# Optimization experiments

Hardware: AMD Instinct MI355X
Metric: run time of the kernel (lower is better)

The kernel has to match this reference:

```python
import jax, jax.numpy as jnp
import numpy as np

N, E, G = 20000, 400000, 200
IN, HID, OUT, H = 8, 64, 32, 4
EPS = 1e-5
NEG_SLOPE = 0.2


def _gatv2(x, src, dst, Wl, bl, Wr, br, att, bias, n, heads, c):
    # lin_l (source messages) and lin_r (target queries)
    xl = (x @ Wl + bl).reshape(n, heads, c)
    xr = (x @ Wr + br).reshape(n, heads, c)
    # per-edge GATv2 score: att . LeakyReLU(x_l[j] + x_r[i])
    e = jax.nn.leaky_relu(xl[src] + xr[dst], NEG_SLOPE)          # [E,H,C]
    score = jnp.einsum('ehc,hc->eh', e, att)                     # [E,H]
    # softmax over incoming edges of each target node
    m = jax.ops.segment_max(score, dst, num_segments=n)
    ex = jnp.exp(score - m[dst])
    den = jax.ops.segment_sum(ex, dst, num_segments=n)
    alpha = ex / den[dst]                                        # [E,H]
    out = jax.ops.segment_sum(alpha[:, :, None] * xl[src], dst, num_segments=n)
    return out.mean(axis=1) + bias                               # concat=False: head mean


def _layernorm(x, g, b):
    mu = x.mean(-1, keepdims=True)
    var = ((x - mu) ** 2).mean(-1, keepdims=True)
    return (x - mu) * jax.lax.rsqrt(var + EPS) * g + b


def setup_inputs() -> dict:
    key = jax.random.key(0)
    ks = jax.random.split(key, 16)
    s = 0.1
    inp = {
        'x': jax.random.normal(ks[0], (N, IN), jnp.float32),
        'edge_index': jax.random.randint(ks[1], (2, E), 0, N, jnp.int64 if jax.config.jax_enable_x64 else jnp.int32),
        'batch': jnp.sort(jax.random.randint(ks[2], (N,), 0, G)),
        'Wl1': jax.random.normal(ks[3], (IN, H * HID), jnp.float32) * s,
        'bl1': jnp.zeros((H * HID,), jnp.float32),
        'Wr1': jax.random.normal(ks[4], (IN, H * HID), jnp.float32) * s,
        'br1': jnp.zeros((H * HID,), jnp.float32),
        'att1': jax.random.normal(ks[5], (H, HID), jnp.float32) * s,
        'b1': jnp.zeros((HID,), jnp.float32),
        'ln1_g': jnp.ones((HID,), jnp.float32),
        'ln1_b': jnp.zeros((HID,), jnp.float32),
        'Wl2': jax.random.normal(ks[6], (HID, H * OUT), jnp.float32) * s,
        'bl2': jnp.zeros((H * OUT,), jnp.float32),
        'Wr2': jax.random.normal(ks[7], (HID, H * OUT), jnp.float32) * s,
        'br2': jnp.zeros((H * OUT,), jnp.float32),
        'att2': jax.random.normal(ks[8], (H, OUT), jnp.float32) * s,
        'b2': jnp.zeros((OUT,), jnp.float32),
        'ln2_g': jnp.ones((OUT,), jnp.float32),
        'ln2_b': jnp.zeros((OUT,), jnp.float32),
    }
    return inp


def reference(x, edge_index, batch, Wl1, bl1, Wr1, br1, att1, b1, ln1_g, ln1_b,
              Wl2, bl2, Wr2, br2, att2, b2, ln2_g, ln2_b):
    n = x.shape[0]
    loop = jnp.arange(n, dtype=edge_index.dtype)  # add_self_loops=True (PyG default)
    src = jnp.concatenate([edge_index[0], loop])
    dst = jnp.concatenate([edge_index[1], loop])

    h = _gatv2(x, src, dst, Wl1, bl1, Wr1, br1, att1, b1, n, H, HID)
    h = jax.nn.relu(_layernorm(h, ln1_g, ln1_b))
    h = _gatv2(h, src, dst, Wl2, bl2, Wr2, br2, att2, b2, n, H, OUT)
    h = jax.nn.relu(_layernorm(h, ln2_g, ln2_b))

    # global mean pool per graph
    cnt = jax.ops.segment_sum(jnp.ones((n,), h.dtype), batch, num_segments=G)
    pooled = jax.ops.segment_sum(h, batch, num_segments=G)
    return pooled / jnp.maximum(cnt, 1.0)[:, None]
```

## Files before the change

### kernel.cpp

```cpp
#include <hip/hip_runtime.h>
#include <math.h>
#include <stdint.h>

#define NEG_SLOPE 0.2f
#define LN_EPS 1e-5f

typedef __attribute__((ext_vector_type(8))) short short8;
typedef __attribute__((ext_vector_type(4))) float f32x4;

__device__ __forceinline__ uint32_t pack_bf2(float a, float b) {
  uint32_t ua = __float_as_uint(a);
  uint32_t ub = __float_as_uint(b);
  ua = (ua + 0x7fffu + ((ua >> 16) & 1u)) >> 16;
  ub = (ub + 0x7fffu + ((ub >> 16) & 1u)) & 0xffff0000u;
  return ua | ub;
}
__device__ __forceinline__ float2 unpack_bf2(uint32_t u) {
  return make_float2(__uint_as_float(u << 16), __uint_as_float(u & 0xffff0000u));
}
__device__ __forceinline__ uint16_t bf16_rne(float f) {
  uint32_t u = __float_as_uint(f);
  return (uint16_t)((u + 0x7fffu + ((u >> 16) & 1u)) >> 16);
}

__device__ __forceinline__ float row16_sum(float x) {
  x += __int_as_float(__builtin_amdgcn_mov_dpp(__float_as_int(x), 0xB1, 0xF, 0xF, true));
  x += __int_as_float(__builtin_amdgcn_mov_dpp(__float_as_int(x), 0x4E, 0xF, 0xF, true));
  x += __int_as_float(__builtin_amdgcn_mov_dpp(__float_as_int(x), 0x124, 0xF, 0xF, true));
  x += __int_as_float(__builtin_amdgcn_mov_dpp(__float_as_int(x), 0x128, 0xF, 0xF, true));
  return x;
}

__global__ void zero_kernel(int* __restrict__ p, int n) {
  int i = blockIdx.x * blockDim.x + threadIdx.x;
  if (i < n) p[i] = 0;
}

__global__ __launch_bounds__(256) void gemm1_hist_kernel(
    const float* __restrict__ x,
    const float* __restrict__ Wl, const float* __restrict__ bl,
    const float* __restrict__ Wr, const float* __restrict__ br,
    uint32_t* __restrict__ xl1b, float* __restrict__ xr1, int N,
    const int* __restrict__ ei, int E, int* __restrict__ cnt) {
  int tid = threadIdx.x;
  int c2 = tid & 127;
  int which = tid >> 7;
  float wl0[8], wl1[8], wr0[8], wr1[8];
#pragma unroll
  for (int k = 0; k < 8; ++k) {
    wl0[k] = Wl[k * 256 + 2 * c2]; wl1[k] = Wl[k * 256 + 2 * c2 + 1];
    wr0[k] = Wr[k * 256 + 2 * c2]; wr1[k] = Wr[k * 256 + 2 * c2 + 1];
  }
  float bl0 = bl[2 * c2], bl1v = bl[2 * c2 + 1];
  float br0 = br[2 * c2], br1v = br[2 * c2 + 1];
  int npair = (N + 1) >> 1;
  for (int pr = blockIdx.x; pr < npair; pr += gridDim.x) {
    int n = pr * 2 + which;
    if (n >= N) continue;
    float4 xa = ((const float4*)x)[n * 2];
    float4 xb = ((const float4*)x)[n * 2 + 1];
    float xs[8] = {xa.x, xa.y, xa.z, xa.w, xb.x, xb.y, xb.z, xb.w};
    float al0 = bl0, al1 = bl1v, ar0 = br0, ar1 = br1v;
#pragma unroll
    for (int k = 0; k < 8; ++k) {
      al0 = fmaf(xs[k], wl0[k], al0); al1 = fmaf(xs[k], wl1[k], al1);
      ar0 = fmaf(xs[k], wr0[k], ar0); ar1 = fmaf(xs[k], wr1[k], ar1);
    }
    xl1b[(size_t)n * 128 + c2] = pack_bf2(al0, al1);
    ((float2*)xr1)[(size_t)n * 128 + c2] = make_float2(ar0, ar1);
  }
  int tot = E + N;
  for (int e = blockIdx.x * blockDim.x + tid; e < tot; e += gridDim.x * blockDim.x) {
    int dst = (e < E) ? ei[E + e] : (e - E);
    atomicAdd(&cnt[dst], 1);
  }
}

__global__ __launch_bounds__(1024) void scan_kernel(const int* __restrict__ cnt,
                                                    int* __restrict__ offs,
                                                    int* __restrict__ cursor, int n) {
  __shared__ int wsum[16];
  int tid = threadIdx.x;
  int lane = tid & 63, w = tid >> 6;
  int PER = (n + 1023) >> 10;
  int base = tid * PER;
  int s = 0;
  for (int j = 0; j < PER; ++j) {
    int idx = base + j;
    s += (idx < n) ? cnt[idx] : 0;
  }
  int inc = s;
#pragma unroll
  for (int d = 1; d < 64; d <<= 1) {
    int t = __shfl_up(inc, d, 64);
    if (lane >= d) inc += t;
  }
  if (lane == 63) wsum[w] = inc;
  __syncthreads();
  int wpre = 0;
  for (int j = 0; j < w; ++j) wpre += wsum[j];
  int run = wpre + inc - s;
  for (int j = 0; j < PER; ++j) {
    int idx = base + j;
    if (idx < n) {
      offs[idx] = run;
      cursor[idx] = run;
      run += cnt[idx];
    }
  }
  if (tid == 1023) offs[n] = run;
}

__global__ void scatter_kernel(const int* __restrict__ ei, int E, int N,
                               int* __restrict__ cursor, int* __restrict__ esrc,
                               const float* __restrict__ Wl2, const float* __restrict__ Wr2,
                               uint16_t* __restrict__ Wtb) {
  if (blockIdx.x < 64) {
    int idx = blockIdx.x * 256 + threadIdx.x;
    int c = idx >> 6, k = idx & 63;
    float v = (c < 128) ? Wl2[k * 128 + c] : Wr2[k * 128 + (c - 128)];
    Wtb[idx] = bf16_rne(v);
  }
  int e = blockIdx.x * blockDim.x + threadIdx.x;
  if (e >= E + N) return;
  int src, dst;
  if (e < E) { src = ei[e]; dst = ei[E + e]; }
  else       { src = e - E; dst = src; }
  int pos = atomicAdd(&cursor[dst], 1);
  esrc[pos] = src;
}

__global__ __launch_bounds__(256) void gemm2_mfma_kernel(
    const uint16_t* __restrict__ h1b,
    const uint16_t* __restrict__ Wtb,
    const float* __restrict__ bl, const float* __restrict__ br,
    uint32_t* __restrict__ xl2b, float* __restrict__ xr2, int N) {
  int lane = threadIdx.x & 63;
  int w = threadIdx.x >> 6;
  int c0 = w << 6;
  int l15 = lane & 15, l4 = lane >> 4;
  int node = (blockIdx.x << 4) + l15;
  int nodec = node < N ? node : N - 1;
  const short8* hrow = (const short8*)(h1b + (size_t)nodec * 64);
  short8 b0 = hrow[l4];
  short8 b1 = hrow[4 + l4];
  f32x4 acc[4] = {{0.f,0.f,0.f,0.f},{0.f,0.f,0.f,0.f},{0.f,0.f,0.f,0.f},{0.f,0.f,0.f,0.f}};
#pragma unroll
  for (int t = 0; t < 4; ++t) {
    int row = c0 + (t << 4) + l15;
    const short8* wrow = (const short8*)(Wtb + (size_t)row * 64);
    short8 a0 = wrow[l4];
    short8 a1 = wrow[4 + l4];
    acc[t] = __builtin_amdgcn_mfma_f32_16x16x32_bf16(a0, b0, acc[t], 0, 0, 0);
    acc[t] = __builtin_amdgcn_mfma_f32_16x16x32_bf16(a1, b1, acc[t], 0, 0, 0);
  }
  if (node >= N) return;
  if (c0 < 128) {
#pragma unroll
    for (int t = 0; t < 4; ++t) {
      int q0 = c0 + (t << 4) + (l4 << 2);
      float4 bb = *(const float4*)(bl + q0);
      uint2 pk;
      pk.x = pack_bf2(acc[t][0] + bb.x, acc[t][1] + bb.y);
      pk.y = pack_bf2(acc[t][2] + bb.z, acc[t][3] + bb.w);
      *(uint2*)(xl2b + (size_t)node * 64 + (q0 >> 1)) = pk;
    }
  } else {
#pragma unroll
    for (int t = 0; t < 4; ++t) {
      int q0 = (c0 - 128) + (t << 4) + (l4 << 2);
      float4 bb = *(const float4*)(br + q0);
      float4 v = make_float4(acc[t][0] + bb.x, acc[t][1] + bb.y,
                             acc[t][2] + bb.z, acc[t][3] + bb.w);
      *(float4*)(xr2 + (size_t)node * 128 + q0) = v;
    }
  }
}

__global__ __launch_bounds__(256) void attn1_kernel(
    const uint32_t* __restrict__ xl1b, const float* __restrict__ xr1,
    const float* __restrict__ att, const float* __restrict__ b1,
    const float* __restrict__ g, const float* __restrict__ be,
    const int* __restrict__ offs, const int* __restrict__ esrc,
    uint32_t* __restrict__ h1b, int N) {
  const float L2E = 1.4426950408889634f;
  int lane = threadIdx.x & 63;
  int i = blockIdx.x * (blockDim.x >> 6) + (threadIdx.x >> 6);
  if (i >= N) return;
  int cq = lane & 15;
  const uint2* xlb = (const uint2*)xl1b;
  float4 attq = ((const float4*)att)[lane];
  float4 a4 = make_float4(0.4f * L2E * attq.x, 0.4f * L2E * attq.y,
                          0.4f * L2E * attq.z, 0.4f * L2E * attq.w);
  float4 xrq = ((const float4*)xr1)[(size_t)i * 64 + lane];
  float dA = 0.f, aA0 = 0.f, aA1 = 0.f, aA2 = 0.f, aA3 = 0.f;
  float dB = 0.f, aB0 = 0.f, aB1 = 0.f, aB2 = 0.f, aB3 = 0.f;
  int beg = offs[i], end = offs[i + 1];
  int p = beg;

#define EDGE1(U, DD, A0, A1, A2, A3)                                           \
  {                                                                            \
    float2 e0 = unpack_bf2(U.x), e1 = unpack_bf2(U.y);                         \
    float t0 = e0.x + xrq.x, t1 = e0.y + xrq.y;                                \
    float t2 = e1.x + xrq.z, t3 = e1.y + xrq.w;                                \
    float u0 = fmaf(1.5f, t0, fabsf(t0));                                      \
    float u1 = fmaf(1.5f, t1, fabsf(t1));                                      \
    float u2 = fmaf(1.5f, t2, fabsf(t2));                                      \
    float u3 = fmaf(1.5f, t3, fabsf(t3));                                      \
    float sc = a4.x * u0;                                                      \
    sc = fmaf(a4.y, u1, sc);                                                   \
    sc = fmaf(a4.z, u2, sc);                                                   \
    sc = fmaf(a4.w, u3, sc);                                                   \
    sc = row16_sum(sc);                                                        \
    float wgt = exp2f(sc);                                                     \
    DD += wgt;                                                                 \
    A0 = fmaf(wgt, e0.x, A0); A1 = fmaf(wgt, e0.y, A1);                        \
    A2 = fmaf(wgt, e1.x, A2); A3 = fmaf(wgt, e1.y, A3);                        \
  }

  for (; p + 3 < end; p += 4) {
    int s0 = __builtin_amdgcn_readfirstlane(esrc[p]);
    int s1 = __builtin_amdgcn_readfirstlane(esrc[p + 1]);
    int s2 = __builtin_amdgcn_readfirstlane(esrc[p + 2]);
    int s3 = __builtin_amdgcn_readfirstlane(esrc[p + 3]);
    uint2 u0 = (xlb + (size_t)s0 * 64)[lane];
    uint2 u1 = (xlb + (size_t)s1 * 64)[lane];
    uint2 u2 = (xlb + (size_t)s2 * 64)[lane];
    uint2 u3 = (xlb + (size_t)s3 * 64)[lane];
    EDGE1(u0, dA, aA0, aA1, aA2, aA3)
    EDGE1(u1, dB, aB0, aB1, aB2, aB3)
    EDGE1(u2, dA, aA0, aA1, aA2, aA3)
    EDGE1(u3, dB, aB0, aB1, aB2, aB3)
  }
  for (; p < end; ++p) {
    int s0 = __builtin_amdgcn_readfirstlane(esrc[p]);
    uint2 u0 = (xlb + (size_t)s0 * 64)[lane];
    EDGE1(u0, dA, aA0, aA1, aA2, aA3)
  }
#undef EDGE1

  float inv = 1.0f / (dA + dB);
  float v0 = (aA0 + aB0) * inv;
  float v1 = (aA1 + aB1) * inv;
  float v2 = (aA2 + aB2) * inv;
  float v3 = (aA3 + aB3) * inv;
  v0 += __shfl_xor(v0, 16, 64); v0 += __shfl_xor(v0, 32, 64);
  v1 += __shfl_xor(v1, 16, 64); v1 += __shfl_xor(v1, 32, 64);
  v2 += __shfl_xor(v2, 16, 64); v2 += __shfl_xor(v2, 32, 64);
  v3 += __shfl_xor(v3, 16, 64); v3 += __shfl_xor(v3, 32, 64);
  float4 b1q = ((const float4*)b1)[cq];
  v0 = 0.25f * v0 + b1q.x;
  v1 = 0.25f * v1 + b1q.y;
  v2 = 0.25f * v2 + b1q.z;
  v3 = 0.25f * v3 + b1q.w;
  float s1 = row16_sum(v0 + v1 + v2 + v3);
  float mu = s1 * (1.0f / 64.0f);
  float d0 = v0 - mu, d1 = v1 - mu, d2 = v2 - mu, d3 = v3 - mu;
  float s2 = row16_sum(d0 * d0 + d1 * d1 + d2 * d2 + d3 * d3);
  float rstd = rsqrtf(s2 * (1.0f / 64.0f) + LN_EPS);
  float4 gq = ((const float4*)g)[cq];
  float4 beq = ((const float4*)be)[cq];
  float y0 = fmaxf(fmaf(d0 * rstd, gq.x, beq.x), 0.f);
  float y1 = fmaxf(fmaf(d1 * rstd, gq.y, beq.y), 0.f);
  float y2 = fmaxf(fmaf(d2 * rstd, gq.z, beq.z), 0.f);
  float y3 = fmaxf(fmaf(d3 * rstd, gq.w, beq.w), 0.f);
  if (lane < 16) {
    uint2 pk;
    pk.x = pack_bf2(y0, y1);
    pk.y = pack_bf2(y2, y3);
    *(uint2*)(h1b + (size_t)i * 32 + cq * 2) = pk;
  }
}

__global__ __launch_bounds__(256) void attn2_kernel(
    const uint32_t* __restrict__ xl2b, const float* __restrict__ xr2,
    const float* __restrict__ att, const float* __restrict__ b2,
    const float* __restrict__ g, const float* __restrict__ be,
    const int* __restrict__ offs, const int* __restrict__ esrc,
    float* __restrict__ h2, int N) {
  const float L2E = 1.4426950408889634f;
  int lane = threadIdx.x & 63;
  int i = blockIdx.x * (blockDim.x >> 6) + (threadIdx.x >> 6);
  if (i >= N) return;
  int cq = lane & 15;
  float2 attq = ((const float2*)att)[lane];
  float2 a4 = make_float2(0.4f * L2E * attq.x, 0.4f * L2E * attq.y);
  float2 xrq = ((const float2*)xr2)[(size_t)i * 64 + lane];
  float dA = 0.f, aA0 = 0.f, aA1 = 0.f;
  float dB = 0.f, aB0 = 0.f, aB1 = 0.f;
  int beg = offs[i], end = offs[i + 1];
  int p = beg;

#define EDGE2(U, DD, A0, A1)                                                   \
  {                                                                            \
    float2 e0 = unpack_bf2(U);                                                 \
    float t0 = e0.x + xrq.x, t1 = e0.y + xrq.y;                                \
    float u0 = fmaf(1.5f, t0, fabsf(t0));                                      \
    float u1 = fmaf(1.5f, t1, fabsf(t1));                                      \
    float sc = fmaf(a4.y, u1, a4.x * u0);                                      \
    sc = row16_sum(sc);                                                        \
    float wgt = exp2f(sc);                                                     \
    DD += wgt;                                                                 \
    A0 = fmaf(wgt, e0.x, A0); A1 = fmaf(wgt, e0.y, A1);                        \
  }

  for (; p + 3 < end; p += 4) {
    int s0 = __builtin_amdgcn_readfirstlane(esrc[p]);
    int s1 = __builtin_amdgcn_readfirstlane(esrc[p + 1]);
    int s2 = __builtin_amdgcn_readfirstlane(esrc[p + 2]);
    int s3 = __builtin_amdgcn_readfirstlane(esrc[p + 3]);
    uint32_t u0 = (xl2b + (size_t)s0 * 64)[lane];
    uint32_t u1 = (xl2b + (size_t)s1 * 64)[lane];
    uint32_t u2 = (xl2b + (size_t)s2 * 64)[lane];
    uint32_t u3 = (xl2b + (size_t)s3 * 64)[lane];
    EDGE2(u0, dA, aA0, aA1)
    EDGE2(u1, dB, aB0, aB1)
    EDGE2(u2, dA, aA0, aA1)
    EDGE2(u3, dB, aB0, aB1)
  }
  for (; p < end; ++p) {
    int s0 = __builtin_amdgcn_readfirstlane(esrc[p]);
    uint32_t u0 = (xl2b + (size_t)s0 * 64)[lane];
    EDGE2(u0, dA, aA0, aA1)
  }
#undef EDGE2

  float inv = 1.0f / (dA + dB);
  float v0 = (aA0 + aB0) * inv;
  float v1 = (aA1 + aB1) * inv;
  v0 += __shfl_xor(v0, 16, 64); v0 += __shfl_xor(v0, 32, 64);
  v1 += __shfl_xor(v1, 16, 64); v1 += __shfl_xor(v1, 32, 64);
  float2 b2q = ((const float2*)b2)[cq];
  v0 = 0.25f * v0 + b2q.x;
  v1 = 0.25f * v1 + b2q.y;
  float s1 = row16_sum(v0 + v1);
  float mu = s1 * (1.0f / 32.0f);
  float d0 = v0 - mu, d1 = v1 - mu;
  float s2 = row16_sum(d0 * d0 + d1 * d1);
  float rstd = rsqrtf(s2 * (1.0f / 32.0f) + LN_EPS);
  float2 gq = ((const float2*)g)[cq];
  float2 beq = ((const float2*)be)[cq];
  float y0 = fmaxf(fmaf(d0 * rstd, gq.x, beq.x), 0.f);
  float y1 = fmaxf(fmaf(d1 * rstd, gq.y, beq.y), 0.f);
  if (lane < 16) ((float2*)h2)[(size_t)i * 16 + cq] = make_float2(y0, y1);
}

__global__ __launch_bounds__(256) void pool_kernel(const float* __restrict__ h2,
                                                   const int* __restrict__ batch,
                                                   float* __restrict__ out, int N) {
  int gidx = blockIdx.x;
  int a = 0, b = N;
  while (a < b) { int m = (a + b) >> 1; if (batch[m] < gidx) a = m + 1; else b = m; }
  int lo = a;
  b = N;
  while (a < b) { int m = (a + b) >> 1; if (batch[m] < gidx + 1) a = m + 1; else b = m; }
  int hi = a;
  int c = threadIdx.x & 31, r = threadIdx.x >> 5;
  float s = 0.f;
  for (int n = lo + r; n < hi; n += 8) s += h2[(size_t)n * 32 + c];
  __shared__ float buf[256];
  buf[threadIdx.x] = s;
  __syncthreads();
  if (threadIdx.x < 128) buf[threadIdx.x] += buf[threadIdx.x + 128];
  __syncthreads();
  if (threadIdx.x < 64) buf[threadIdx.x] += buf[threadIdx.x + 64];
  __syncthreads();
  if (threadIdx.x < 32) {
    float v = buf[threadIdx.x] + buf[threadIdx.x + 32];
    int cnt = hi - lo;
    out[gidx * 32 + threadIdx.x] = v / (float)(cnt > 0 ? cnt : 1);
  }
}

extern "C" void kernel_launch(void* const* d_in, const int* in_sizes, int n_in,
                              void* d_out, int out_size, void* d_ws, size_t ws_size,
                              hipStream_t stream) {
  const float* x    = (const float*)d_in[0];
  const int*   ei   = (const int*)d_in[1];
  const int*   batch= (const int*)d_in[2];
  const float* Wl1  = (const float*)d_in[3];
  const float* bl1  = (const float*)d_in[4];
  const float* Wr1  = (const float*)d_in[5];
  const float* br1  = (const float*)d_in[6];
  const float* att1 = (const float*)d_in[7];
  const float* b1   = (const float*)d_in[8];
  const float* ln1g = (const float*)d_in[9];
  const float* ln1b = (const float*)d_in[10];
  const float* Wl2  = (const float*)d_in[11];
  const float* bl2  = (const float*)d_in[12];
  const float* Wr2  = (const float*)d_in[13];
  const float* br2  = (const float*)d_in[14];
  const float* att2 = (const float*)d_in[15];
  const float* b2   = (const float*)d_in[16];
  const float* ln2g = (const float*)d_in[17];
  const float* ln2b = (const float*)d_in[18];

  int N = in_sizes[0] / 8;
  int E = in_sizes[1] / 2;
  int G = out_size / 32;

  char* ws = (char*)d_ws;
  size_t off = 0;
  auto alloc = [&](size_t bytes) -> void* {
    void* p = (void*)(ws + off);
    off += (bytes + 255) & ~(size_t)255;
    return p;
  };
  int*      cnt    = (int*)alloc((size_t)N * 4);
  int*      offs   = (int*)alloc((size_t)(N + 1) * 4);
  int*      cursor = (int*)alloc((size_t)N * 4);
  int*      esrc   = (int*)alloc((size_t)(E + N) * 4);
  uint32_t* xl1b   = (uint32_t*)alloc((size_t)N * 128 * 4);
  float*    xr1    = (float*)alloc((size_t)N * 256 * 4);
  uint32_t* h1b    = (uint32_t*)alloc((size_t)N * 64 * 2);
  uint16_t* Wtb    = (uint16_t*)alloc((size_t)256 * 64 * 2);
  uint32_t* xl2b   = (uint32_t*)alloc((size_t)N * 64 * 4);
  float*    xr2    = (float*)alloc((size_t)N * 128 * 4);
  float*    h2     = (float*)alloc((size_t)N * 32 * 4);

  int tot = E + N;
  zero_kernel<<<(N + 255) / 256, 256, 0, stream>>>(cnt, N);
  gemm1_hist_kernel<<<2048, 256, 0, stream>>>(x, Wl1, bl1, Wr1, br1, xl1b, xr1, N,
                                              ei, E, cnt);
  scan_kernel<<<1, 1024, 0, stream>>>(cnt, offs, cursor, N);
  scatter_kernel<<<(tot + 255) / 256, 256, 0, stream>>>(ei, E, N, cursor, esrc,
                                                        Wl2, Wr2, Wtb);

  attn1_kernel<<<(N + 3) / 4, 256, 0, stream>>>(xl1b, xr1, att1, b1, ln1g, ln1b,
                                                offs, esrc, h1b, N);
  gemm2_mfma_kernel<<<(N + 15) / 16, 256, 0, stream>>>((const uint16_t*)h1b, Wtb, bl2, br2,
                                                       xl2b, xr2, N);
  attn2_kernel<<<(N + 3) / 4, 256, 0, stream>>>(xl2b, xr2, att2, b2, ln2g, ln2b,
                                                offs, esrc, h2, N);

  pool_kernel<<<G, 256, 0, stream>>>(h2, batch, (float*)d_out, N);
}
```

Baseline: 175.8 us.

## Fuse layer-1 projection into attention gather and pool via atomics

```diff
diff --git a/kernel.cpp b/kernel.cpp
--- a/kernel.cpp
+++ b/kernel.cpp
@@ -36,44 +36,11 @@
   if (i < n) p[i] = 0;
 }
 
-__global__ __launch_bounds__(256) void gemm1_hist_kernel(
-    const float* __restrict__ x,
-    const float* __restrict__ Wl, const float* __restrict__ bl,
-    const float* __restrict__ Wr, const float* __restrict__ br,
-    uint32_t* __restrict__ xl1b, float* __restrict__ xr1, int N,
-    const int* __restrict__ ei, int E, int* __restrict__ cnt) {
-  int tid = threadIdx.x;
-  int c2 = tid & 127;
-  int which = tid >> 7;
-  float wl0[8], wl1[8], wr0[8], wr1[8];
-#pragma unroll
-  for (int k = 0; k < 8; ++k) {
-    wl0[k] = Wl[k * 256 + 2 * c2]; wl1[k] = Wl[k * 256 + 2 * c2 + 1];
-    wr0[k] = Wr[k * 256 + 2 * c2]; wr1[k] = Wr[k * 256 + 2 * c2 + 1];
-  }
-  float bl0 = bl[2 * c2], bl1v = bl[2 * c2 + 1];
-  float br0 = br[2 * c2], br1v = br[2 * c2 + 1];
-  int npair = (N + 1) >> 1;
-  for (int pr = blockIdx.x; pr < npair; pr += gridDim.x) {
-    int n = pr * 2 + which;
-    if (n >= N) continue;
-    float4 xa = ((const float4*)x)[n * 2];
-    float4 xb = ((const float4*)x)[n * 2 + 1];
-    float xs[8] = {xa.x, xa.y, xa.z, xa.w, xb.x, xb.y, xb.z, xb.w};
-    float al0 = bl0, al1 = bl1v, ar0 = br0, ar1 = br1v;
-#pragma unroll
-    for (int k = 0; k < 8; ++k) {
-      al0 = fmaf(xs[k], wl0[k], al0); al1 = fmaf(xs[k], wl1[k], al1);
-      ar0 = fmaf(xs[k], wr0[k], ar0); ar1 = fmaf(xs[k], wr1[k], ar1);
-    }
-    xl1b[(size_t)n * 128 + c2] = pack_bf2(al0, al1);
-    ((float2*)xr1)[(size_t)n * 128 + c2] = make_float2(ar0, ar1);
-  }
-  int tot = E + N;
-  for (int e = blockIdx.x * blockDim.x + tid; e < tot; e += gridDim.x * blockDim.x) {
-    int dst = (e < E) ? ei[E + e] : (e - E);
-    atomicAdd(&cnt[dst], 1);
-  }
+__global__ void hist_kernel(const int* __restrict__ ei, int E, int N, int* __restrict__ cnt) {
+  int e = blockIdx.x * blockDim.x + threadIdx.x;
+  if (e >= E + N) return;
+  int dst = (e < E) ? ei[E + e] : (e - E);
+  atomicAdd(&cnt[dst], 1);
 }
 
 __global__ __launch_bounds__(1024) void scan_kernel(const int* __restrict__ cnt,
@@ -178,7 +145,9 @@
 }
 
 __global__ __launch_bounds__(256) void attn1_kernel(
-    const uint32_t* __restrict__ xl1b, const float* __restrict__ xr1,
+    const float* __restrict__ x,
+    const float* __restrict__ Wl, const float* __restrict__ bl,
+    const float* __restrict__ Wr, const float* __restrict__ br,
     const float* __restrict__ att, const float* __restrict__ b1,
     const float* __restrict__ g, const float* __restrict__ be,
     const int* __restrict__ offs, const int* __restrict__ esrc,
@@ -188,25 +157,50 @@
   int i = blockIdx.x * (blockDim.x >> 6) + (threadIdx.x >> 6);
   if (i >= N) return;
   int cq = lane & 15;
-  const uint2* xlb = (const uint2*)xl1b;
+  const float4* xf4 = (const float4*)x;
+  float4 wl[8];
+#pragma unroll
+  for (int k = 0; k < 8; ++k) wl[k] = ((const float4*)(Wl + k * 256))[lane];
   float4 attq = ((const float4*)att)[lane];
   float4 a4 = make_float4(0.4f * L2E * attq.x, 0.4f * L2E * attq.y,
                           0.4f * L2E * attq.z, 0.4f * L2E * attq.w);
-  float4 xrq = ((const float4*)xr1)[(size_t)i * 64 + lane];
-  float dA = 0.f, aA0 = 0.f, aA1 = 0.f, aA2 = 0.f, aA3 = 0.f;
-  float dB = 0.f, aB0 = 0.f, aB1 = 0.f, aB2 = 0.f, aB3 = 0.f;
+  float4 xa = xf4[(size_t)i * 2], xbv = xf4[(size_t)i * 2 + 1];
+  float xs[8] = {xa.x, xa.y, xa.z, xa.w, xbv.x, xbv.y, xbv.z, xbv.w};
+  float4 xr = ((const float4*)br)[lane];
+#pragma unroll
+  for (int k = 0; k < 8; ++k) {
+    float4 wr = ((const float4*)(Wr + k * 256))[lane];
+    xr.x = fmaf(xs[k], wr.x, xr.x);
+    xr.y = fmaf(xs[k], wr.y, xr.y);
+    xr.z = fmaf(xs[k], wr.z, xr.z);
+    xr.w = fmaf(xs[k], wr.w, xr.w);
+  }
+  float4 tb = ((const float4*)bl)[lane];
+  tb.x += xr.x; tb.y += xr.y; tb.z += xr.z; tb.w += xr.w;
+
+  float dA = 0.f, dB = 0.f;
+  float4 accA = make_float4(0.f, 0.f, 0.f, 0.f);
+  float4 accB = make_float4(0.f, 0.f, 0.f, 0.f);
   int beg = offs[i], end = offs[i + 1];
   int p = beg;
 
-#define EDGE1(U, DD, A0, A1, A2, A3)                                           \
+#define EDGE1(XA, XB, DD, ACC)                                                 \
   {                                                                            \
-    float2 e0 = unpack_bf2(U.x), e1 = unpack_bf2(U.y);                         \
-    float t0 = e0.x + xrq.x, t1 = e0.y + xrq.y;                                \
-    float t2 = e1.x + xrq.z, t3 = e1.y + xrq.w;                                \
-    float u0 = fmaf(1.5f, t0, fabsf(t0));                                      \
-    float u1 = fmaf(1.5f, t1, fabsf(t1));                                      \
-    float u2 = fmaf(1.5f, t2, fabsf(t2));                                      \
-    float u3 = fmaf(1.5f, t3, fabsf(t3));                                      \
+    float ks0 = XA.x, ks1 = XA.y, ks2 = XA.z, ks3 = XA.w;                      \
+    float ks4 = XB.x, ks5 = XB.y, ks6 = XB.z, ks7 = XB.w;                      \
+    float kk[8] = {ks0, ks1, ks2, ks3, ks4, ks5, ks6, ks7};                    \
+    float4 t = tb;                                                             \
+    _Pragma("unroll")                                                          \
+    for (int k = 0; k < 8; ++k) {                                              \
+      t.x = fmaf(kk[k], wl[k].x, t.x);                                         \
+      t.y = fmaf(kk[k], wl[k].y, t.y);                                         \
+      t.z = fmaf(kk[k], wl[k].z, t.z);                                         \
+      t.w = fmaf(kk[k], wl[k].w, t.w);                                         \
+    }                                                                          \
+    float u0 = fmaf(1.5f, t.x, fabsf(t.x));                                    \
+    float u1 = fmaf(1.5f, t.y, fabsf(t.y));                                    \
+    float u2 = fmaf(1.5f, t.z, fabsf(t.z));                                    \
+    float u3 = fmaf(1.5f, t.w, fabsf(t.w));                                    \
     float sc = a4.x * u0;                                                      \
     sc = fmaf(a4.y, u1, sc);                                                   \
     sc = fmaf(a4.z, u2, sc);                                                   \
@@ -214,8 +208,10 @@
     sc = row16_sum(sc);                                                        \
     float wgt = exp2f(sc);                                                     \
     DD += wgt;                                                                 \
-    A0 = fmaf(wgt, e0.x, A0); A1 = fmaf(wgt, e0.y, A1);                        \
-    A2 = fmaf(wgt, e1.x, A2); A3 = fmaf(wgt, e1.y, A3);                        \
+    ACC.x = fmaf(wgt, t.x, ACC.x);                                             \
+    ACC.y = fmaf(wgt, t.y, ACC.y);                                             \
+    ACC.z = fmaf(wgt, t.z, ACC.z);                                             \
+    ACC.w = fmaf(wgt, t.w, ACC.w);                                             \
   }
 
   for (; p + 3 < end; p += 4) {
@@ -223,27 +219,27 @@
     int s1 = __builtin_amdgcn_readfirstlane(esrc[p + 1]);
     int s2 = __builtin_amdgcn_readfirstlane(esrc[p + 2]);
     int s3 = __builtin_amdgcn_readfirstlane(esrc[p + 3]);
-    uint2 u0 = (xlb + (size_t)s0 * 64)[lane];
-    uint2 u1 = (xlb + (size_t)s1 * 64)[lane];
-    uint2 u2 = (xlb + (size_t)s2 * 64)[lane];
-    uint2 u3 = (xlb + (size_t)s3 * 64)[lane];
-    EDGE1(u0, dA, aA0, aA1, aA2, aA3)
-    EDGE1(u1, dB, aB0, aB1, aB2, aB3)
-    EDGE1(u2, dA, aA0, aA1, aA2, aA3)
-    EDGE1(u3, dB, aB0, aB1, aB2, aB3)
+    float4 xa0 = xf4[(size_t)s0 * 2], xb0 = xf4[(size_t)s0 * 2 + 1];
+    float4 xa1 = xf4[(size_t)s1 * 2], xb1 = xf4[(size_t)s1 * 2 + 1];
+    float4 xa2 = xf4[(size_t)s2 * 2], xb2 = xf4[(size_t)s2 * 2 + 1];
+    float4 xa3 = xf4[(size_t)s3 * 2], xb3 = xf4[(size_t)s3 * 2 + 1];
+    EDGE1(xa0, xb0, dA, accA)
+    EDGE1(xa1, xb1, dB, accB)
+    EDGE1(xa2, xb2, dA, accA)
+    EDGE1(xa3, xb3, dB, accB)
   }
   for (; p < end; ++p) {
     int s0 = __builtin_amdgcn_readfirstlane(esrc[p]);
-    uint2 u0 = (xlb + (size_t)s0 * 64)[lane];
-    EDGE1(u0, dA, aA0, aA1, aA2, aA3)
+    float4 xa0 = xf4[(size_t)s0 * 2], xb0 = xf4[(size_t)s0 * 2 + 1];
+    EDGE1(xa0, xb0, dA, accA)
   }
 #undef EDGE1
 
   float inv = 1.0f / (dA + dB);
-  float v0 = (aA0 + aB0) * inv;
-  float v1 = (aA1 + aB1) * inv;
-  float v2 = (aA2 + aB2) * inv;
-  float v3 = (aA3 + aB3) * inv;
+  float v0 = (accA.x + accB.x) * inv - xr.x;
+  float v1 = (accA.y + accB.y) * inv - xr.y;
+  float v2 = (accA.z + accB.z) * inv - xr.z;
+  float v3 = (accA.w + accB.w) * inv - xr.w;
   v0 += __shfl_xor(v0, 16, 64); v0 += __shfl_xor(v0, 32, 64);
   v1 += __shfl_xor(v1, 16, 64); v1 += __shfl_xor(v1, 32, 64);
   v2 += __shfl_xor(v2, 16, 64); v2 += __shfl_xor(v2, 32, 64);
@@ -277,7 +273,7 @@
     const float* __restrict__ att, const float* __restrict__ b2,
     const float* __restrict__ g, const float* __restrict__ be,
     const int* __restrict__ offs, const int* __restrict__ esrc,
-    float* __restrict__ h2, int N) {
+    const int* __restrict__ batch, float* __restrict__ pooled, int N) {
   const float L2E = 1.4426950408889634f;
   int lane = threadIdx.x & 63;
   int i = blockIdx.x * (blockDim.x >> 6) + (threadIdx.x >> 6);
@@ -342,34 +338,24 @@
   float2 beq = ((const float2*)be)[cq];
   float y0 = fmaxf(fmaf(d0 * rstd, gq.x, beq.x), 0.f);
   float y1 = fmaxf(fmaf(d1 * rstd, gq.y, beq.y), 0.f);
-  if (lane < 16) ((float2*)h2)[(size_t)i * 16 + cq] = make_float2(y0, y1);
-}
-
-__global__ __launch_bounds__(256) void pool_kernel(const float* __restrict__ h2,
-                                                   const int* __restrict__ batch,
-                                                   float* __restrict__ out, int N) {
+  if (lane < 16) {
+    int gi = batch[i];
+    atomicAdd(&pooled[gi * 32 + 2 * cq], y0);
+    atomicAdd(&pooled[gi * 32 + 2 * cq + 1], y1);
+  }
+}
+
+__global__ void final_kernel(const float* __restrict__ pooled, const int* __restrict__ batch,
+                             float* __restrict__ out, int N) {
   int gidx = blockIdx.x;
   int a = 0, b = N;
   while (a < b) { int m = (a + b) >> 1; if (batch[m] < gidx) a = m + 1; else b = m; }
   int lo = a;
   b = N;
   while (a < b) { int m = (a + b) >> 1; if (batch[m] < gidx + 1) a = m + 1; else b = m; }
-  int hi = a;
-  int c = threadIdx.x & 31, r = threadIdx.x >> 5;
-  float s = 0.f;
-  for (int n = lo + r; n < hi; n += 8) s += h2[(size_t)n * 32 + c];
-  __shared__ float buf[256];
-  buf[threadIdx.x] = s;
-  __syncthreads();
-  if (threadIdx.x < 128) buf[threadIdx.x] += buf[threadIdx.x + 128];
-  __syncthreads();
-  if (threadIdx.x < 64) buf[threadIdx.x] += buf[threadIdx.x + 64];
-  __syncthreads();
-  if (threadIdx.x < 32) {
-    float v = buf[threadIdx.x] + buf[threadIdx.x + 32];
-    int cnt = hi - lo;
-    out[gidx * 32 + threadIdx.x] = v / (float)(cnt > 0 ? cnt : 1);
-  }
+  int cntv = a - lo;
+  float inv = 1.0f / (float)(cntv > 0 ? cntv : 1);
+  out[gidx * 32 + threadIdx.x] = pooled[gidx * 32 + threadIdx.x] * inv;
 }
 
 extern "C" void kernel_launch(void* const* d_in, const int* in_sizes, int n_in,
@@ -407,31 +393,29 @@
     return p;
   };
   int*      cnt    = (int*)alloc((size_t)N * 4);
+  float*    pooled = (float*)alloc((size_t)G * 32 * 4);
   int*      offs   = (int*)alloc((size_t)(N + 1) * 4);
   int*      cursor = (int*)alloc((size_t)N * 4);
   int*      esrc   = (int*)alloc((size_t)(E + N) * 4);
-  uint32_t* xl1b   = (uint32_t*)alloc((size_t)N * 128 * 4);
-  float*    xr1    = (float*)alloc((size_t)N * 256 * 4);
   uint32_t* h1b    = (uint32_t*)alloc((size_t)N * 64 * 2);
   uint16_t* Wtb    = (uint16_t*)alloc((size_t)256 * 64 * 2);
   uint32_t* xl2b   = (uint32_t*)alloc((size_t)N * 64 * 4);
   float*    xr2    = (float*)alloc((size_t)N * 128 * 4);
-  float*    h2     = (float*)alloc((size_t)N * 32 * 4);
-
+
+  int zero_ints = (int)(((char*)(pooled + (size_t)G * 32) - (char*)cnt) / 4);
   int tot = E + N;
-  zero_kernel<<<(N + 255) / 256, 256, 0, stream>>>(cnt, N);
-  gemm1_hist_kernel<<<2048, 256, 0, stream>>>(x, Wl1, bl1, Wr1, br1, xl1b, xr1, N,
-                                              ei, E, cnt);
+  zero_kernel<<<(zero_ints + 255) / 256, 256, 0, stream>>>(cnt, zero_ints);
+  hist_kernel<<<(tot + 255) / 256, 256, 0, stream>>>(ei, E, N, cnt);
   scan_kernel<<<1, 1024, 0, stream>>>(cnt, offs, cursor, N);
   scatter_kernel<<<(tot + 255) / 256, 256, 0, stream>>>(ei, E, N, cursor, esrc,
                                                         Wl2, Wr2, Wtb);
 
-  attn1_kernel<<<(N + 3) / 4, 256, 0, stream>>>(xl1b, xr1, att1, b1, ln1g, ln1b,
-                                                offs, esrc, h1b, N);
+  attn1_kernel<<<(N + 3) / 4, 256, 0, stream>>>(x, Wl1, bl1, Wr1, br1, att1, b1,
+                                                ln1g, ln1b, offs, esrc, h1b, N);
   gemm2_mfma_kernel<<<(N + 15) / 16, 256, 0, stream>>>((const uint16_t*)h1b, Wtb, bl2, br2,
                                                        xl2b, xr2, N);
   attn2_kernel<<<(N + 3) / 4, 256, 0, stream>>>(xl2b, xr2, att2, b2, ln2g, ln2b,
-                                                offs, esrc, h2, N);
-
-  pool_kernel<<<G, 256, 0, stream>>>(h2, batch, (float*)d_out, N);
-}
+                                                offs, esrc, batch, pooled, N);
+
+  final_kernel<<<G, 32, 0, stream>>>(pooled, batch, (float*)d_out, N);
+}
```

Result: slower. 187.3 us (+6.5%).
